# Kernel tuning notes

Hardware: AMD Instinct MI355X
Metric: run time of the kernel (lower is better)

The kernel has to match this reference:

```python
import jax, jax.numpy as jnp
import numpy as np

NUM_EXPERTS = 8
HIDDEN = 2048
INTER = 4096
TOKENS = 8192
TOP_K = 2


def setup_inputs() -> dict:
    key = jax.random.key(0)
    ks = jax.random.split(key, 5)
    s = 0.02
    return {
        "x": jax.random.normal(ks[0], (TOKENS, HIDDEN), dtype=jnp.float32),
        "gate_w": jax.random.normal(ks[1], (NUM_EXPERTS, HIDDEN), dtype=jnp.float32) * s,
        "w1": jax.random.normal(ks[2], (NUM_EXPERTS, INTER, HIDDEN), dtype=jnp.float32) * s,
        "w2": jax.random.normal(ks[3], (NUM_EXPERTS, HIDDEN, INTER), dtype=jnp.float32) * s,
        "w3": jax.random.normal(ks[4], (NUM_EXPERTS, INTER, HIDDEN), dtype=jnp.float32) * s,
    }


def reference(x, gate_w, w1, w2, w3):
    # Router: softmax over experts in fp32, then top-2 (no renormalization,
    # matching the torch module which uses the raw top-k softmax probs).
    router_logits = jnp.einsum("th,eh->te", x, gate_w)  # [T, E]
    probs = jax.nn.softmax(router_logits.astype(jnp.float32), axis=1)
    topk_w, topk_idx = jax.lax.top_k(probs, TOP_K)  # [T, K]
    topk_w = topk_w.astype(x.dtype)

    num_experts = w1.shape[0]
    out = jnp.zeros_like(x)
    for e in range(num_experts):
        # Combined routing coefficient for expert e per token (0 if unrouted).
        coef = jnp.sum(jnp.where(topk_idx == e, topk_w, 0.0), axis=1)  # [T]
        # SwiGLU expert FFN: down(silu(gate(x)) * up(x))
        g = jnp.einsum("th,ih->ti", x, w1[e])
        u = jnp.einsum("th,ih->ti", x, w3[e])
        h = jax.nn.silu(g) * u
        y = jnp.einsum("ti,hi->th", h, w2[e])
        out = out + coef[:, None] * y
    return out
```

## Files before the change

kernel.cpp:

```cpp
#include <hip/hip_runtime.h>
#include <stdint.h>
#include <stddef.h>


constexpr int kTokens  = 8192;
constexpr int kHidden  = 2048;
constexpr int kInter   = 4096;
constexpr int kExperts = 8;

constexpr int BM = 128, BN = 128, BK = 64;
constexpr int MAX_MT = (2 * kTokens) / BM + kExperts;

constexpr int BM2 = 256, BN2 = 128, BK2 = 64;
constexpr int MAX_MT2 = (2 * kTokens) / BM2 + kExperts;
constexpr int NT2 = kHidden / BK2;

typedef short bf16x8 __attribute__((ext_vector_type(8)));
typedef float f32x4  __attribute__((ext_vector_type(4)));
typedef unsigned int u32;

__device__ __forceinline__ unsigned short f2bf(float f) {
  union { float f; unsigned u; } v; v.f = f;
  unsigned r = v.u + 0x7FFFu + ((v.u >> 16) & 1u);
  return (unsigned short)(r >> 16);
}

__device__ __forceinline__ void gload16(const void* g, void* l) {
  __builtin_amdgcn_global_load_lds(
      (const __attribute__((address_space(1))) u32*)g,
      (__attribute__((address_space(3))) u32*)l, 16, 0, 0);
}

__global__ __launch_bounds__(256) void convert_w(
    const float* __restrict__ src, unsigned short* __restrict__ dst,
    int lp, int lq, int K, long nchunks)
{
  long stride = (long)gridDim.x * blockDim.x;
  for (long g = blockIdx.x * (long)blockDim.x + threadIdx.x; g < nchunks; g += stride) {
    int  l   = (int)(g & 1023);
    long blk = g >> 10;
    int  q   = (int)(blk & ((1 << lq) - 1));
    long ep  = blk >> lq;
    int  p   = (int)(ep & ((1 << lp) - 1));
    int  e   = (int)(ep >> lp);
    int r = l >> 3, cs = l & 7, c = cs ^ (r & 7);
    size_t soff = (((size_t)(e << lp) + p) * 128 + r) * (size_t)K + (size_t)q * 64 + c * 8;
    float4 v0 = *reinterpret_cast<const float4*>(src + soff);
    float4 v1 = *reinterpret_cast<const float4*>(src + soff + 4);
    uint4 o;
    o.x = (u32)f2bf(v0.x) | ((u32)f2bf(v0.y) << 16);
    o.y = (u32)f2bf(v0.z) | ((u32)f2bf(v0.w) << 16);
    o.z = (u32)f2bf(v1.x) | ((u32)f2bf(v1.y) << 16);
    o.w = (u32)f2bf(v1.z) | ((u32)f2bf(v1.w) << 16);
    *reinterpret_cast<uint4*>(dst + g * 8) = o;
  }
}

__global__ __launch_bounds__(256) void moe_router(
    const float* __restrict__ x, const float* __restrict__ gate_w,
    unsigned short* __restrict__ xb, int* __restrict__ counts,
    int* __restrict__ list_idx, float* __restrict__ list_w)
{
  const int lane = threadIdx.x & 63;
  const int wave = threadIdx.x >> 6;
  const int t = blockIdx.x * 4 + wave;

  float acc[kExperts];
#pragma unroll
  for (int e = 0; e < kExperts; ++e) acc[e] = 0.f;

  const float4* xrow = reinterpret_cast<const float4*>(x + (size_t)t * kHidden);
#pragma unroll
  for (int j = 0; j < 8; ++j) {
    float4 xv = xrow[j * 64 + lane];
    uint2 pk;
    pk.x = (u32)f2bf(xv.x) | ((u32)f2bf(xv.y) << 16);
    pk.y = (u32)f2bf(xv.z) | ((u32)f2bf(xv.w) << 16);
    *reinterpret_cast<uint2*>(xb + (size_t)t * kHidden + j * 256 + lane * 4) = pk;
#pragma unroll
    for (int e = 0; e < kExperts; ++e) {
      float4 gv = reinterpret_cast<const float4*>(gate_w + (size_t)e * kHidden)[j * 64 + lane];
      acc[e] += xv.x * gv.x + xv.y * gv.y + xv.z * gv.z + xv.w * gv.w;
    }
  }
#pragma unroll
  for (int e = 0; e < kExperts; ++e) {
#pragma unroll
    for (int m = 32; m >= 1; m >>= 1) acc[e] += __shfl_xor(acc[e], m);
  }
  if (lane == 0) {
    float mx = acc[0];
#pragma unroll
    for (int e = 1; e < kExperts; ++e) mx = fmaxf(mx, acc[e]);
    float p[kExperts]; float s = 0.f;
#pragma unroll
    for (int e = 0; e < kExperts; ++e) { p[e] = __expf(acc[e] - mx); s += p[e]; }
    float inv = 1.f / s;
    int i1 = 0; float v1 = p[0];
#pragma unroll
    for (int e = 1; e < kExperts; ++e) if (p[e] > v1) { v1 = p[e]; i1 = e; }
    int i2 = (i1 == 0) ? 1 : 0; float v2 = p[i2];
#pragma unroll
    for (int e = 0; e < kExperts; ++e) {
      if (e == i1 || e == i2) continue;
      if (p[e] > v2) { v2 = p[e]; i2 = e; }
    }
    int s1 = atomicAdd(&counts[i1], 1);
    list_idx[i1 * kTokens + s1] = t;
    list_w [i1 * kTokens + s1] = v1 * inv;
    int s2 = atomicAdd(&counts[i2], 1);
    list_idx[i2 * kTokens + s2] = t;
    list_w [i2 * kTokens + s2] = v2 * inv;
  }
}

__device__ __forceinline__ bool map_tile(const int* __restrict__ counts, int mt,
                                         int& e, int& lm, int& sb, int& ne)
{
  int tb = 0; sb = 0;
  for (e = 0; e < kExperts; ++e) {
    ne = counts[e];
    int tiles = (ne + BM - 1) / BM;
    if (mt < tb + tiles) { lm = mt - tb; return true; }
    tb += tiles; sb += ne;
  }
  return false;
}

__device__ __forceinline__ bool map_tile2(const int* __restrict__ counts, int mt,
                                          int& e, int& lm, int& sb, int& ne)
{
  int tb = 0; sb = 0;
  for (e = 0; e < kExperts; ++e) {
    ne = counts[e];
    int tiles = (ne + BM2 - 1) / BM2;
    if (mt < tb + tiles) { lm = mt - tb; return true; }
    tb += tiles; sb += ne;
  }
  return false;
}

__global__ __launch_bounds__(512, 2) void moe_gu2(
    const unsigned short* __restrict__ xb,
    const unsigned short* __restrict__ w1b, const unsigned short* __restrict__ w3b,
    const int* __restrict__ counts, const int* __restrict__ list_idx,
    unsigned short* __restrict__ hbuf)
{
  __shared__ unsigned short lds[65536];
  __shared__ int toks[BM2];

  const int tid = threadIdx.x;
  const int nt  = blockIdx.x / MAX_MT2;
  const int mt  = blockIdx.x % MAX_MT2;

  int e, lm, sb, ne;
  if (!map_tile2(counts, mt, e, lm, sb, ne)) return;
  const int row0 = lm * BM2;

  if (tid < BM2) {
    int lr = row0 + tid;
    toks[tid] = list_idx[e * kTokens + ((lr < ne) ? lr : 0)];
  }
  __syncthreads();

  const int lane = tid & 63;
  const int w    = tid >> 6;
  const int wr   = w >> 2;
  const int wc   = w & 3;

  const unsigned short* srcA[2][2];
  const unsigned short* srcB1[2];
  const unsigned short* srcB3[2];
  {
    const size_t bb = ((size_t)(e * (kInter / BN2) + nt) * (kHidden / BK2)) * 1024;
#pragma unroll
    for (int i = 0; i < 2; ++i) {
      int l = (w * 2 + i) * 64 + lane;
      int r = l >> 3, cs = l & 7, c = cs ^ (r & 7);
#pragma unroll
      for (int h = 0; h < 2; ++h)
        srcA[h][i] = xb + (size_t)toks[h * 128 + r] * kHidden + c * 8;
      srcB1[i] = w1b + (bb + l) * 8;
      srcB3[i] = w3b + (bb + l) * 8;
    }
  }

  f32x4 accG[8][2], accU[8][2];
  const f32x4 zero = {0.f, 0.f, 0.f, 0.f};
#pragma unroll
  for (int m = 0; m < 8; ++m)
#pragma unroll
    for (int n = 0; n < 2; ++n) { accG[m][n] = zero; accU[m][n] = zero; }

#pragma unroll
  for (int i = 0; i < 2; ++i) gload16(srcA[0][i], &lds[0 * 8192 + (w * 2 + i) * 512]);
#pragma unroll
  for (int i = 0; i < 2; ++i) gload16(srcA[1][i], &lds[1 * 8192 + (w * 2 + i) * 512]);
#pragma unroll
  for (int i = 0; i < 2; ++i) gload16(srcB1[i], &lds[32768 + (w * 2 + i) * 512]);
#pragma unroll
  for (int i = 0; i < 2; ++i) gload16(srcB3[i], &lds[49152 + (w * 2 + i) * 512]);
  asm volatile("s_waitcnt vmcnt(2)" ::: "memory");
  __builtin_amdgcn_sched_barrier(0);
  __builtin_amdgcn_s_barrier();

  for (int t = 0; t < NT2; ++t) {
    const int cb = t & 1, nb = cb ^ 1;
    const int tn = (t + 1 < NT2) ? (t + 1) : (NT2 - 1);
    const int Acur = (cb * 2 + wr) * 8192;
    const int B1c  = 32768 + cb * 8192;
    const int B3c  = 49152 + cb * 8192;
    const int An0  = (nb * 2 + 0) * 8192;
    const int An1  = (nb * 2 + 1) * 8192;
    const int B1n  = 32768 + nb * 8192;
    const int B3n  = 49152 + nb * 8192;

    bf16x8 a0[4][2], a1[4][2];
    {
      bf16x8 b1f[2][2];
#pragma unroll
      for (int m = 0; m < 4; ++m) {
        const int r = m * 16 + (lane & 15);
#pragma unroll
        for (int kk = 0; kk < 2; ++kk) {
          const int cq = kk * 4 + (lane >> 4);
          a0[m][kk] = *reinterpret_cast<const bf16x8*>(&lds[Acur + r * 64 + ((cq ^ (r & 7)) << 3)]);
        }
      }
#pragma unroll
      for (int n = 0; n < 2; ++n) {
        const int r = wc * 32 + n * 16 + (lane & 15);
#pragma unroll
        for (int kk = 0; kk < 2; ++kk) {
          const int cq = kk * 4 + (lane >> 4);
          b1f[n][kk] = *reinterpret_cast<const bf16x8*>(&lds[B1c + r * 64 + ((cq ^ (r & 7)) << 3)]);
        }
      }
#pragma unroll
      for (int i = 0; i < 2; ++i) gload16(srcA[0][i] + tn * 64, &lds[An0 + (w * 2 + i) * 512]);
      __builtin_amdgcn_s_setprio(1);
#pragma unroll
      for (int m = 0; m < 4; ++m)
#pragma unroll
        for (int n = 0; n < 2; ++n)
#pragma unroll
          for (int kk = 0; kk < 2; ++kk)
            accG[m][n] = __builtin_amdgcn_mfma_f32_16x16x32_bf16(a0[m][kk], b1f[n][kk], accG[m][n], 0, 0, 0);
      __builtin_amdgcn_s_setprio(0);
      __builtin_amdgcn_sched_barrier(0);
      __builtin_amdgcn_s_barrier();

#pragma unroll
      for (int m = 0; m < 4; ++m) {
        const int r = 64 + m * 16 + (lane & 15);
#pragma unroll
        for (int kk = 0; kk < 2; ++kk) {
          const int cq = kk * 4 + (lane >> 4);
          a1[m][kk] = *reinterpret_cast<const bf16x8*>(&lds[Acur + r * 64 + ((cq ^ (r & 7)) << 3)]);
        }
      }
#pragma unroll
      for (int i = 0; i < 2; ++i) gload16(srcA[1][i] + tn * 64, &lds[An1 + (w * 2 + i) * 512]);
      __builtin_amdgcn_s_setprio(1);
#pragma unroll
      for (int m = 0; m < 4; ++m)
#pragma unroll
        for (int n = 0; n < 2; ++n)
#pragma unroll
          for (int kk = 0; kk < 2; ++kk)
            accG[4 + m][n] = __builtin_amdgcn_mfma_f32_16x16x32_bf16(a1[m][kk], b1f[n][kk], accG[4 + m][n], 0, 0, 0);
      __builtin_amdgcn_s_setprio(0);
      __builtin_amdgcn_sched_barrier(0);
      asm volatile("s_waitcnt vmcnt(4)" ::: "memory");
      __builtin_amdgcn_s_barrier();
    }
    {
      bf16x8 b3f[2][2];
#pragma unroll
      for (int n = 0; n < 2; ++n) {
        const int r = wc * 32 + n * 16 + (lane & 15);
#pragma unroll
        for (int kk = 0; kk < 2; ++kk) {
          const int cq = kk * 4 + (lane >> 4);
          b3f[n][kk] = *reinterpret_cast<const bf16x8*>(&lds[B3c + r * 64 + ((cq ^ (r & 7)) << 3)]);
        }
      }
#pragma unroll
      for (int i = 0; i < 2; ++i) gload16(srcB1[i] + (size_t)tn * 8192, &lds[B1n + (w * 2 + i) * 512]);
      __builtin_amdgcn_s_setprio(1);
#pragma unroll
      for (int m = 0; m < 4; ++m)
#pragma unroll
        for (int n = 0; n < 2; ++n)
#pragma unroll
          for (int kk = 0; kk < 2; ++kk)
            accU[m][n] = __builtin_amdgcn_mfma_f32_16x16x32_bf16(a0[m][kk], b3f[n][kk], accU[m][n], 0, 0, 0);
      __builtin_amdgcn_s_setprio(0);
      __builtin_amdgcn_sched_barrier(0);
      __builtin_amdgcn_s_barrier();

#pragma unroll
      for (int i = 0; i < 2; ++i) gload16(srcB3[i] + (size_t)tn * 8192, &lds[B3n + (w * 2 + i) * 512]);
      __builtin_amdgcn_s_setprio(1);
#pragma unroll
      for (int m = 0; m < 4; ++m)
#pragma unroll
        for (int n = 0; n < 2; ++n)
#pragma unroll
          for (int kk = 0; kk < 2; ++kk)
            accU[4 + m][n] = __builtin_amdgcn_mfma_f32_16x16x32_bf16(a1[m][kk], b3f[n][kk], accU[4 + m][n], 0, 0, 0);
      __builtin_amdgcn_s_setprio(0);
      __builtin_amdgcn_sched_barrier(0);
      asm volatile("s_waitcnt vmcnt(2)" ::: "memory");
      __builtin_amdgcn_s_barrier();
    }
  }

#pragma unroll
  for (int am = 0; am < 8; ++am) {
#pragma unroll
    for (int r = 0; r < 4; ++r) {
      int rloc = wr * 128 + am * 16 + ((lane >> 4) * 4) + r;
      int lrow = row0 + rloc;
      if (lrow < ne) {
        size_t base = (size_t)(sb + lrow) * kInter + (size_t)nt * BN2 + wc * 32 + (lane & 15);
#pragma unroll
        for (int n = 0; n < 2; ++n) {
          float g = accG[am][n][r];
          float u = accU[am][n][r];
          float hv = (g / (1.f + __expf(-g))) * u;
          hbuf[base + n * 16] = f2bf(hv);
        }
      }
    }
  }
}

__global__ __launch_bounds__(256, 3) void moe_y(
    const unsigned short* __restrict__ hbuf,
    const unsigned short* __restrict__ w2b,
    const int* __restrict__ counts, const int* __restrict__ list_idx,
    const float* __restrict__ list_w,
    float* __restrict__ out)
{
  __shared__ unsigned short As[BM * BK];
  __shared__ unsigned short Bs[BN * BK];
  __shared__ int   toks[BM];
  __shared__ float cofs[BM];

  const int tid = threadIdx.x;
  const int nt  = blockIdx.x / MAX_MT;
  const int mt  = blockIdx.x % MAX_MT;

  int e, lm, sb, ne;
  if (!map_tile(counts, mt, e, lm, sb, ne)) return;
  const int row0 = lm * BM;

  if (tid < BM) {
    int lr = row0 + tid;
    bool v = lr < ne;
    toks[tid] = v ? list_idx[e * kTokens + lr] : 0;
    cofs[tid] = v ? list_w [e * kTokens + lr] : 0.f;
  }
  __syncthreads();

  const int lane = tid & 63;
  const int w = tid >> 6;
  const int wr = w >> 1, wc = w & 1;

  const unsigned short* srcA[4];
  const unsigned short* srcB2[4];
  const size_t bbase = ((size_t)(e * (kHidden / BN) + nt) * (kInter / BK)) * 1024;
#pragma unroll
  for (int i = 0; i < 4; ++i) {
    int l = (w * 4 + i) * 64 + lane;
    int r = l >> 3, cs = l & 7, c = cs ^ (r & 7);
    srcA[i]  = hbuf + (size_t)(sb + row0 + r) * kInter + c * 8;
    srcB2[i] = w2b  + (bbase + l) * 8;
  }

  f32x4 acc[4][4];
  const f32x4 zero = {0.f, 0.f, 0.f, 0.f};
#pragma unroll
  for (int m = 0; m < 4; ++m)
#pragma unroll
    for (int n = 0; n < 4; ++n) acc[m][n] = zero;

  for (int ks = 0; ks < kInter / BK; ++ks) {
#pragma unroll
    for (int i = 0; i < 4; ++i) {
      gload16(srcA[i]  + ks * BK,           &As[(w * 4 + i) * 512]);
      gload16(srcB2[i] + (size_t)ks * 8192, &Bs[(w * 4 + i) * 512]);
    }
    __syncthreads();
#pragma unroll
    for (int kk = 0; kk < 2; ++kk) {
      const int cq = kk * 4 + (lane >> 4);
      bf16x8 a[4], b[4];
#pragma unroll
      for (int m = 0; m < 4; ++m) {
        int row = wr * 64 + m * 16 + (lane & 15);
        a[m] = *reinterpret_cast<const bf16x8*>(&As[row * 64 + ((cq ^ (row & 7)) << 3)]);
      }
#pragma unroll
      for (int n = 0; n < 4; ++n) {
        int row = wc * 64 + n * 16 + (lane & 15);
        b[n] = *reinterpret_cast<const bf16x8*>(&Bs[row * 64 + ((cq ^ (row & 7)) << 3)]);
      }
#pragma unroll
      for (int m = 0; m < 4; ++m)
#pragma unroll
        for (int n = 0; n < 4; ++n)
          acc[m][n] = __builtin_amdgcn_mfma_f32_16x16x32_bf16(a[m], b[n], acc[m][n], 0, 0, 0);
    }
    __syncthreads();
  }

#pragma unroll
  for (int m = 0; m < 4; ++m) {
#pragma unroll
    for (int r = 0; r < 4; ++r) {
      int rloc = wr * 64 + m * 16 + ((lane >> 4) * 4) + r;
      if (row0 + rloc < ne) {
        float cf = cofs[rloc];
        size_t obase = (size_t)toks[rloc] * kHidden + (size_t)nt * BN + wc * 64 + (lane & 15);
#pragma unroll
        for (int n = 0; n < 4; ++n)
          atomicAdd(&out[obase + n * 16], cf * acc[m][n][r]);
      }
    }
  }
}

__global__ __launch_bounds__(256, 2) void moe_gu_f32(
    const unsigned short* __restrict__ xb,
    const float* __restrict__ w1, const float* __restrict__ w3,
    const int* __restrict__ counts, const int* __restrict__ list_idx,
    unsigned short* __restrict__ hbuf)
{
  __shared__ unsigned short As [BM * BK];
  __shared__ unsigned short B1s[BN * BK];
  __shared__ unsigned short B3s[BN * BK];
  __shared__ int toks[BM];

  const int tid = threadIdx.x;
  const int nt  = blockIdx.x / MAX_MT;
  const int mt  = blockIdx.x % MAX_MT;

  int e, lm, sb, ne;
  if (!map_tile(counts, mt, e, lm, sb, ne)) return;
  const int row0 = lm * BM;

  if (tid < BM) {
    int lr = row0 + tid;
    toks[tid] = list_idx[e * kTokens + ((lr < ne) ? lr : 0)];
  }
  __syncthreads();

  const unsigned short* aptr[4];
#pragma unroll
  for (int i = 0; i < 4; ++i) {
    int chunk = i * 256 + tid;
    int r = chunk >> 3, c8 = chunk & 7;
    aptr[i] = xb + (size_t)toks[r] * kHidden + c8 * 8;
  }
  const float* w1e = w1 + (size_t)e * kInter * kHidden;
  const float* w3e = w3 + (size_t)e * kInter * kHidden;

  f32x4 accG[4][4], accU[4][4];
  const f32x4 zero = {0.f, 0.f, 0.f, 0.f};
#pragma unroll
  for (int m = 0; m < 4; ++m)
#pragma unroll
    for (int n = 0; n < 4; ++n) { accG[m][n] = zero; accU[m][n] = zero; }

  const int lane = tid & 63;
  const int wr = (tid >> 6) >> 1;
  const int wc = (tid >> 6) & 1;

  for (int k0 = 0; k0 < kHidden; k0 += BK) {
#pragma unroll
    for (int i = 0; i < 4; ++i) {
      int chunk = i * 256 + tid;
      uint4 v = *reinterpret_cast<const uint4*>(aptr[i] + k0);
      *reinterpret_cast<uint4*>(&As[chunk * 8]) = v;
    }
#pragma unroll
    for (int i = 0; i < 8; ++i) {
      int c = i * 256 + tid;
      int rowB = c >> 4, c16 = c & 15;
      size_t off = ((size_t)(nt * BN + rowB)) * kHidden + k0 + c16 * 4;
      float4 v1 = *reinterpret_cast<const float4*>(w1e + off);
      float4 v3 = *reinterpret_cast<const float4*>(w3e + off);
      uint2 p1, p3;
      p1.x = (u32)f2bf(v1.x) | ((u32)f2bf(v1.y) << 16);
      p1.y = (u32)f2bf(v1.z) | ((u32)f2bf(v1.w) << 16);
      p3.x = (u32)f2bf(v3.x) | ((u32)f2bf(v3.y) << 16);
      p3.y = (u32)f2bf(v3.z) | ((u32)f2bf(v3.w) << 16);
      *reinterpret_cast<uint2*>(&B1s[rowB * BK + c16 * 4]) = p1;
      *reinterpret_cast<uint2*>(&B3s[rowB * BK + c16 * 4]) = p3;
    }
    __syncthreads();
#pragma unroll
    for (int kk = 0; kk < 2; ++kk) {
      const int klo = kk * 32 + (lane >> 4) * 8;
      bf16x8 a[4], b1v[4], b3v[4];
#pragma unroll
      for (int m = 0; m < 4; ++m)
        a[m] = *reinterpret_cast<const bf16x8*>(&As[(wr * 64 + m * 16 + (lane & 15)) * BK + klo]);
#pragma unroll
      for (int n = 0; n < 4; ++n) {
        b1v[n] = *reinterpret_cast<const bf16x8*>(&B1s[(wc * 64 + n * 16 + (lane & 15)) * BK + klo]);
        b3v[n] = *reinterpret_cast<const bf16x8*>(&B3s[(wc * 64 + n * 16 + (lane & 15)) * BK + klo]);
      }
#pragma unroll
      for (int m = 0; m < 4; ++m)
#pragma unroll
        for (int n = 0; n < 4; ++n) {
          accG[m][n] = __builtin_amdgcn_mfma_f32_16x16x32_bf16(a[m], b1v[n], accG[m][n], 0, 0, 0);
          accU[m][n] = __builtin_amdgcn_mfma_f32_16x16x32_bf16(a[m], b3v[n], accU[m][n], 0, 0, 0);
        }
    }
    __syncthreads();
  }
#pragma unroll
  for (int m = 0; m < 4; ++m) {
#pragma unroll
    for (int r = 0; r < 4; ++r) {
      int rloc = wr * 64 + m * 16 + ((lane >> 4) * 4) + r;
      int lrow = row0 + rloc;
      if (lrow < ne) {
        size_t base = (size_t)(sb + lrow) * kInter + (size_t)nt * BN + wc * 64 + (lane & 15);
#pragma unroll
        for (int n = 0; n < 4; ++n) {
          float g = accG[m][n][r];
          float u = accU[m][n][r];
          hbuf[base + n * 16] = f2bf((g / (1.f + __expf(-g))) * u);
        }
      }
    }
  }
}

__global__ __launch_bounds__(256, 2) void moe_y_f32(
    const unsigned short* __restrict__ hbuf,
    const float* __restrict__ w2,
    const int* __restrict__ counts, const int* __restrict__ list_idx,
    const float* __restrict__ list_w,
    float* __restrict__ out)
{
  __shared__ unsigned short As[BM * BK];
  __shared__ unsigned short Bs[BN * BK];
  __shared__ int   toks[BM];
  __shared__ float cofs[BM];

  const int tid = threadIdx.x;
  const int nt  = blockIdx.x / MAX_MT;
  const int mt  = blockIdx.x % MAX_MT;

  int e, lm, sb, ne;
  if (!map_tile(counts, mt, e, lm, sb, ne)) return;
  const int row0 = lm * BM;

  if (tid < BM) {
    int lr = row0 + tid;
    bool v = lr < ne;
    toks[tid] = v ? list_idx[e * kTokens + lr] : 0;
    cofs[tid] = v ? list_w [e * kTokens + lr] : 0.f;
  }
  __syncthreads();

  const float* w2e = w2 + (size_t)e * kHidden * kInter;
  const unsigned short* arow = hbuf + (size_t)(sb + row0) * kInter;

  f32x4 acc[4][4];
  const f32x4 zero = {0.f, 0.f, 0.f, 0.f};
#pragma unroll
  for (int m = 0; m < 4; ++m)
#pragma unroll
    for (int n = 0; n < 4; ++n) acc[m][n] = zero;

  const int lane = tid & 63;
  const int wr = (tid >> 6) >> 1;
  const int wc = (tid >> 6) & 1;

  for (int k0 = 0; k0 < kInter; k0 += BK) {
#pragma unroll
    for (int i = 0; i < 4; ++i) {
      int chunk = i * 256 + tid;
      int r = chunk >> 3, c8 = chunk & 7;
      uint4 v = *reinterpret_cast<const uint4*>(arow + (size_t)r * kInter + k0 + c8 * 8);
      *reinterpret_cast<uint4*>(&As[chunk * 8]) = v;
    }
#pragma unroll
    for (int i = 0; i < 8; ++i) {
      int c = i * 256 + tid;
      int rowB = c >> 4, c16 = c & 15;
      size_t off = ((size_t)(nt * BN + rowB)) * kInter + k0 + c16 * 4;
      float4 v2 = *reinterpret_cast<const float4*>(w2e + off);
      uint2 p2;
      p2.x = (u32)f2bf(v2.x) | ((u32)f2bf(v2.y) << 16);
      p2.y = (u32)f2bf(v2.z) | ((u32)f2bf(v2.w) << 16);
      *reinterpret_cast<uint2*>(&Bs[rowB * BK + c16 * 4]) = p2;
    }
    __syncthreads();
#pragma unroll
    for (int kk = 0; kk < 2; ++kk) {
      const int klo = kk * 32 + (lane >> 4) * 8;
      bf16x8 a[4], b[4];
#pragma unroll
      for (int m = 0; m < 4; ++m)
        a[m] = *reinterpret_cast<const bf16x8*>(&As[(wr * 64 + m * 16 + (lane & 15)) * BK + klo]);
#pragma unroll
      for (int n = 0; n < 4; ++n)
        b[n] = *reinterpret_cast<const bf16x8*>(&Bs[(wc * 64 + n * 16 + (lane & 15)) * BK + klo]);
#pragma unroll
      for (int m = 0; m < 4; ++m)
#pragma unroll
        for (int n = 0; n < 4; ++n)
          acc[m][n] = __builtin_amdgcn_mfma_f32_16x16x32_bf16(a[m], b[n], acc[m][n], 0, 0, 0);
    }
    __syncthreads();
  }
#pragma unroll
  for (int m = 0; m < 4; ++m) {
#pragma unroll
    for (int r = 0; r < 4; ++r) {
      int rloc = wr * 64 + m * 16 + ((lane >> 4) * 4) + r;
      if (row0 + rloc < ne) {
        float cf = cofs[rloc];
        size_t obase = (size_t)toks[rloc] * kHidden + (size_t)nt * BN + wc * 64 + (lane & 15);
#pragma unroll
        for (int n = 0; n < 4; ++n)
          atomicAdd(&out[obase + n * 16], cf * acc[m][n][r]);
      }
    }
  }
}

extern "C" void kernel_launch(void* const* d_in, const int* in_sizes, int n_in,
                              void* d_out, int out_size, void* d_ws, size_t ws_size,
                              hipStream_t stream)
{
  const float* x      = (const float*)d_in[0];
  const float* gate_w = (const float*)d_in[1];
  const float* w1     = (const float*)d_in[2];
  const float* w2     = (const float*)d_in[3];
  const float* w3     = (const float*)d_in[4];
  float* out = (float*)d_out;

  char* ws = (char*)d_ws;
  const size_t MiB = 1ull << 20;
  int*   counts   = (int*)(ws);
  int*   list_idx = (int*)(ws + 1024);
  float* list_w   = (float*)(ws + 1024 + kExperts * kTokens * 4);

  hipMemsetAsync(counts, 0, 1024, stream);
  hipMemsetAsync(out, 0, (size_t)kTokens * kHidden * sizeof(float), stream);

  if (ws_size >= 418 * MiB) {
    unsigned short* xb   = (unsigned short*)(ws + 1 * MiB);
    unsigned short* w1b  = (unsigned short*)(ws + 33 * MiB);
    unsigned short* w3b  = (unsigned short*)(ws + 161 * MiB);
    unsigned short* hbuf = (unsigned short*)(ws + 289 * MiB);
    unsigned short* w2b  = w1b;

    const long nch = (long)kExperts * (kInter / BN) * (kHidden / BK) * 1024;
    convert_w<<<4096, 256, 0, stream>>>(w1, w1b, 5, 5, kHidden, nch);
    convert_w<<<4096, 256, 0, stream>>>(w3, w3b, 5, 5, kHidden, nch);
    moe_router<<<kTokens / 4, 256, 0, stream>>>(x, gate_w, xb, counts, list_idx, list_w);
    moe_gu2<<<(kInter / BN2) * MAX_MT2, 512, 0, stream>>>(xb, w1b, w3b, counts, list_idx, hbuf);
    convert_w<<<4096, 256, 0, stream>>>(w2, w2b, 4, 6, kInter, nch);
    moe_y<<<(kHidden / BN) * MAX_MT, 256, 0, stream>>>(hbuf, w2b, counts, list_idx, list_w, out);
  } else {
    unsigned short* xb   = (unsigned short*)(ws + 1 * MiB);
    unsigned short* hbuf = (unsigned short*)(ws + 36 * MiB);
    moe_router<<<kTokens / 4, 256, 0, stream>>>(x, gate_w, xb, counts, list_idx, list_w);
    moe_gu_f32<<<(kInter / BN) * MAX_MT, 256, 0, stream>>>(xb, w1, w3, counts, list_idx, hbuf);
    moe_y_f32 <<<(kHidden / BN) * MAX_MT, 256, 0, stream>>>(hbuf, w2, counts, list_idx, list_w, out);
  }
}
```

Baseline: 1.492 ms.

## Restructure gate/up and down-projection kernels with staggered prefetch pipeline and larger down tiles

```diff
diff --git a/kernel.cpp b/kernel.cpp
--- a/kernel.cpp
+++ b/kernel.cpp
@@ -11,9 +11,13 @@
 constexpr int BM = 128, BN = 128, BK = 64;
 constexpr int MAX_MT = (2 * kTokens) / BM + kExperts;
 
-constexpr int BM2 = 256, BN2 = 128, BK2 = 64;
+constexpr int BM2 = 256;
 constexpr int MAX_MT2 = (2 * kTokens) / BM2 + kExperts;
-constexpr int NT2 = kHidden / BK2;
+constexpr int NT2 = kHidden / BK;
+constexpr int NTY = kInter / BK;
+constexpr int NPAN_GU = kInter / 128;
+constexpr int NPAN_Y  = kHidden / 256;
+constexpr int kSlotCap = 16512;
 
 typedef short bf16x8 __attribute__((ext_vector_type(8)));
 typedef float f32x4  __attribute__((ext_vector_type(4)));
@@ -30,6 +34,11 @@
       (const __attribute__((address_space(1))) u32*)g,
       (__attribute__((address_space(3))) u32*)l, 16, 0, 0);
 }
+
+#define SB0()    __builtin_amdgcn_sched_barrier(0)
+#define BAR()    __builtin_amdgcn_s_barrier()
+#define LGKM0()  asm volatile("s_waitcnt lgkmcnt(0)" ::: "memory")
+#define VM(N)    asm volatile("s_waitcnt vmcnt(" #N ")" ::: "memory")
 
 __global__ __launch_bounds__(256) void convert_w(
     const float* __restrict__ src, unsigned short* __restrict__ dst,
@@ -140,7 +149,7 @@
   return false;
 }
 
-__global__ __launch_bounds__(512, 2) void moe_gu2(
+__global__ __launch_bounds__(512, 2) void moe_gu4(
     const unsigned short* __restrict__ xb,
     const unsigned short* __restrict__ w1b, const unsigned short* __restrict__ w3b,
     const int* __restrict__ counts, const int* __restrict__ list_idx,
@@ -169,21 +178,18 @@
   const int wc   = w & 3;
 
   const unsigned short* srcA[2][2];
-  const unsigned short* srcB1[2];
-  const unsigned short* srcB3[2];
-  {
-    const size_t bb = ((size_t)(e * (kInter / BN2) + nt) * (kHidden / BK2)) * 1024;
-#pragma unroll
-    for (int i = 0; i < 2; ++i) {
-      int l = (w * 2 + i) * 64 + lane;
-      int r = l >> 3, cs = l & 7, c = cs ^ (r & 7);
-#pragma unroll
-      for (int h = 0; h < 2; ++h)
-        srcA[h][i] = xb + (size_t)toks[h * 128 + r] * kHidden + c * 8;
-      srcB1[i] = w1b + (bb + l) * 8;
-      srcB3[i] = w3b + (bb + l) * 8;
-    }
-  }
+  int cOff[2];
+#pragma unroll
+  for (int j = 0; j < 2; ++j) {
+    int l = (w * 2 + j) * 64 + lane;
+    int r = l >> 3, c = (l & 7) ^ (r & 7);
+#pragma unroll
+    for (int h = 0; h < 2; ++h)
+      srcA[h][j] = xb + (size_t)toks[h * 128 + r] * kHidden + c * 8;
+    cOff[j] = l * 8;
+  }
+  const unsigned short* pB1 = w1b + (size_t)(e * NPAN_GU + nt) * NT2 * 8192;
+  const unsigned short* pB3 = w3b + (size_t)(e * NPAN_GU + nt) * NT2 * 8192;
 
   f32x4 accG[8][2], accU[8][2];
   const f32x4 zero = {0.f, 0.f, 0.f, 0.f};
@@ -192,52 +198,57 @@
 #pragma unroll
     for (int n = 0; n < 2; ++n) { accG[m][n] = zero; accU[m][n] = zero; }
 
-#pragma unroll
-  for (int i = 0; i < 2; ++i) gload16(srcA[0][i], &lds[0 * 8192 + (w * 2 + i) * 512]);
-#pragma unroll
-  for (int i = 0; i < 2; ++i) gload16(srcA[1][i], &lds[1 * 8192 + (w * 2 + i) * 512]);
-#pragma unroll
-  for (int i = 0; i < 2; ++i) gload16(srcB1[i], &lds[32768 + (w * 2 + i) * 512]);
-#pragma unroll
-  for (int i = 0; i < 2; ++i) gload16(srcB3[i], &lds[49152 + (w * 2 + i) * 512]);
-  asm volatile("s_waitcnt vmcnt(2)" ::: "memory");
-  __builtin_amdgcn_sched_barrier(0);
-  __builtin_amdgcn_s_barrier();
-
-  for (int t = 0; t < NT2; ++t) {
-    const int cb = t & 1, nb = cb ^ 1;
-    const int tn = (t + 1 < NT2) ? (t + 1) : (NT2 - 1);
-    const int Acur = (cb * 2 + wr) * 8192;
-    const int B1c  = 32768 + cb * 8192;
-    const int B3c  = 49152 + cb * 8192;
-    const int An0  = (nb * 2 + 0) * 8192;
-    const int An1  = (nb * 2 + 1) * 8192;
-    const int B1n  = 32768 + nb * 8192;
-    const int B3n  = 49152 + nb * 8192;
-
-    bf16x8 a0[4][2], a1[4][2];
-    {
-      bf16x8 b1f[2][2];
+  const int dA = (w * 2) * 512;
+
+#pragma unroll
+  for (int j = 0; j < 2; ++j) gload16(pB1 + cOff[j], &lds[32768 + dA + j * 512]);
+#pragma unroll
+  for (int j = 0; j < 2; ++j) gload16(pB3 + cOff[j], &lds[49152 + dA + j * 512]);
+#pragma unroll
+  for (int j = 0; j < 2; ++j) gload16(srcA[0][j], &lds[0 + dA + j * 512]);
+#pragma unroll
+  for (int j = 0; j < 2; ++j) gload16(srcA[1][j], &lds[8192 + dA + j * 512]);
+#pragma unroll
+  for (int j = 0; j < 2; ++j) gload16(srcA[0][j] + BK, &lds[16384 + dA + j * 512]);
+#pragma unroll
+  for (int j = 0; j < 2; ++j) gload16(srcA[1][j] + BK, &lds[24576 + dA + j * 512]);
+  SB0(); VM(4); SB0(); BAR();
+
+  for (int s2 = 0; s2 < NT2; s2 += 2) {
+#pragma unroll
+    for (int u = 0; u < 2; ++u) {
+      const int s  = s2 + u;
+      const int b  = u, nb = u ^ 1;
+      const int sp1 = (s + 1 < NT2) ? (s + 1) : (NT2 - 1);
+      const int sp2 = (s + 2 < NT2) ? (s + 2) : (NT2 - 1);
+      const int aub = b * 16384 + wr * 8192;
+      const int b1b = 32768 + b * 8192;
+      const int b3b = 49152 + b * 8192;
+
+      bf16x8 a0[4][2], a1[4][2], b1f[2][2], b3f[2][2];
+
 #pragma unroll
       for (int m = 0; m < 4; ++m) {
-        const int r = m * 16 + (lane & 15);
+        const int rr = m * 16 + (lane & 15);
 #pragma unroll
         for (int kk = 0; kk < 2; ++kk) {
           const int cq = kk * 4 + (lane >> 4);
-          a0[m][kk] = *reinterpret_cast<const bf16x8*>(&lds[Acur + r * 64 + ((cq ^ (r & 7)) << 3)]);
+          a0[m][kk] = *reinterpret_cast<const bf16x8*>(&lds[aub + rr * 64 + ((cq ^ (rr & 7)) << 3)]);
         }
       }
 #pragma unroll
       for (int n = 0; n < 2; ++n) {
-        const int r = wc * 32 + n * 16 + (lane & 15);
+        const int rr = wc * 32 + n * 16 + (lane & 15);
 #pragma unroll
         for (int kk = 0; kk < 2; ++kk) {
           const int cq = kk * 4 + (lane >> 4);
-          b1f[n][kk] = *reinterpret_cast<const bf16x8*>(&lds[B1c + r * 64 + ((cq ^ (r & 7)) << 3)]);
-        }
-      }
-#pragma unroll
-      for (int i = 0; i < 2; ++i) gload16(srcA[0][i] + tn * 64, &lds[An0 + (w * 2 + i) * 512]);
+          b1f[n][kk] = *reinterpret_cast<const bf16x8*>(&lds[b1b + rr * 64 + ((cq ^ (rr & 7)) << 3)]);
+        }
+      }
+#pragma unroll
+      for (int j = 0; j < 2; ++j)
+        gload16(pB1 + (size_t)sp1 * 8192 + cOff[j], &lds[32768 + nb * 8192 + dA + j * 512]);
+      SB0(); BAR(); LGKM0(); SB0();
       __builtin_amdgcn_s_setprio(1);
 #pragma unroll
       for (int m = 0; m < 4; ++m)
@@ -247,20 +258,21 @@
           for (int kk = 0; kk < 2; ++kk)
             accG[m][n] = __builtin_amdgcn_mfma_f32_16x16x32_bf16(a0[m][kk], b1f[n][kk], accG[m][n], 0, 0, 0);
       __builtin_amdgcn_s_setprio(0);
-      __builtin_amdgcn_sched_barrier(0);
-      __builtin_amdgcn_s_barrier();
+      SB0(); BAR();
 
 #pragma unroll
       for (int m = 0; m < 4; ++m) {
-        const int r = 64 + m * 16 + (lane & 15);
+        const int rr = 64 + m * 16 + (lane & 15);
 #pragma unroll
         for (int kk = 0; kk < 2; ++kk) {
           const int cq = kk * 4 + (lane >> 4);
-          a1[m][kk] = *reinterpret_cast<const bf16x8*>(&lds[Acur + r * 64 + ((cq ^ (r & 7)) << 3)]);
-        }
-      }
-#pragma unroll
-      for (int i = 0; i < 2; ++i) gload16(srcA[1][i] + tn * 64, &lds[An1 + (w * 2 + i) * 512]);
+          a1[m][kk] = *reinterpret_cast<const bf16x8*>(&lds[aub + rr * 64 + ((cq ^ (rr & 7)) << 3)]);
+        }
+      }
+#pragma unroll
+      for (int j = 0; j < 2; ++j)
+        gload16(pB3 + (size_t)sp1 * 8192 + cOff[j], &lds[49152 + nb * 8192 + dA + j * 512]);
+      SB0(); BAR(); LGKM0(); SB0();
       __builtin_amdgcn_s_setprio(1);
 #pragma unroll
       for (int m = 0; m < 4; ++m)
@@ -270,23 +282,21 @@
           for (int kk = 0; kk < 2; ++kk)
             accG[4 + m][n] = __builtin_amdgcn_mfma_f32_16x16x32_bf16(a1[m][kk], b1f[n][kk], accG[4 + m][n], 0, 0, 0);
       __builtin_amdgcn_s_setprio(0);
-      __builtin_amdgcn_sched_barrier(0);
-      asm volatile("s_waitcnt vmcnt(4)" ::: "memory");
-      __builtin_amdgcn_s_barrier();
-    }
-    {
-      bf16x8 b3f[2][2];
+      SB0(); VM(8); BAR();
+
 #pragma unroll
       for (int n = 0; n < 2; ++n) {
-        const int r = wc * 32 + n * 16 + (lane & 15);
+        const int rr = wc * 32 + n * 16 + (lane & 15);
 #pragma unroll
         for (int kk = 0; kk < 2; ++kk) {
           const int cq = kk * 4 + (lane >> 4);
-          b3f[n][kk] = *reinterpret_cast<const bf16x8*>(&lds[B3c + r * 64 + ((cq ^ (r & 7)) << 3)]);
-        }
-      }
-#pragma unroll
-      for (int i = 0; i < 2; ++i) gload16(srcB1[i] + (size_t)tn * 8192, &lds[B1n + (w * 2 + i) * 512]);
+          b3f[n][kk] = *reinterpret_cast<const bf16x8*>(&lds[b3b + rr * 64 + ((cq ^ (rr & 7)) << 3)]);
+        }
+      }
+#pragma unroll
+      for (int j = 0; j < 2; ++j)
+        gload16(srcA[0][j] + sp2 * BK, &lds[b * 16384 + dA + j * 512]);
+      SB0(); BAR(); LGKM0(); SB0();
       __builtin_amdgcn_s_setprio(1);
 #pragma unroll
       for (int m = 0; m < 4; ++m)
@@ -296,11 +306,12 @@
           for (int kk = 0; kk < 2; ++kk)
             accU[m][n] = __builtin_amdgcn_mfma_f32_16x16x32_bf16(a0[m][kk], b3f[n][kk], accU[m][n], 0, 0, 0);
       __builtin_amdgcn_s_setprio(0);
-      __builtin_amdgcn_sched_barrier(0);
-      __builtin_amdgcn_s_barrier();
-
-#pragma unroll
-      for (int i = 0; i < 2; ++i) gload16(srcB3[i] + (size_t)tn * 8192, &lds[B3n + (w * 2 + i) * 512]);
+      SB0(); BAR();
+
+#pragma unroll
+      for (int j = 0; j < 2; ++j)
+        gload16(srcA[1][j] + sp2 * BK, &lds[b * 16384 + 8192 + dA + j * 512]);
+      SB0(); BAR(); LGKM0(); SB0();
       __builtin_amdgcn_s_setprio(1);
 #pragma unroll
       for (int m = 0; m < 4; ++m)
@@ -310,9 +321,7 @@
           for (int kk = 0; kk < 2; ++kk)
             accU[4 + m][n] = __builtin_amdgcn_mfma_f32_16x16x32_bf16(a1[m][kk], b3f[n][kk], accU[4 + m][n], 0, 0, 0);
       __builtin_amdgcn_s_setprio(0);
-      __builtin_amdgcn_sched_barrier(0);
-      asm volatile("s_waitcnt vmcnt(2)" ::: "memory");
-      __builtin_amdgcn_s_barrier();
+      SB0(); VM(6); BAR();
     }
   }
 
@@ -323,7 +332,7 @@
       int rloc = wr * 128 + am * 16 + ((lane >> 4) * 4) + r;
       int lrow = row0 + rloc;
       if (lrow < ne) {
-        size_t base = (size_t)(sb + lrow) * kInter + (size_t)nt * BN2 + wc * 32 + (lane & 15);
+        size_t base = (size_t)(sb + lrow) * kInter + (size_t)nt * 128 + wc * 32 + (lane & 15);
 #pragma unroll
         for (int n = 0; n < 2; ++n) {
           float g = accG[am][n][r];
@@ -336,27 +345,26 @@
   }
 }
 
-__global__ __launch_bounds__(256, 3) void moe_y(
+__global__ __launch_bounds__(512, 2) void moe_y4(
     const unsigned short* __restrict__ hbuf,
     const unsigned short* __restrict__ w2b,
     const int* __restrict__ counts, const int* __restrict__ list_idx,
     const float* __restrict__ list_w,
     float* __restrict__ out)
 {
-  __shared__ unsigned short As[BM * BK];
-  __shared__ unsigned short Bs[BN * BK];
-  __shared__ int   toks[BM];
-  __shared__ float cofs[BM];
+  __shared__ unsigned short lds[65536];
+  __shared__ int   toks[BM2];
+  __shared__ float cofs[BM2];
 
   const int tid = threadIdx.x;
-  const int nt  = blockIdx.x / MAX_MT;
-  const int mt  = blockIdx.x % MAX_MT;
+  const int nt  = blockIdx.x / MAX_MT2;
+  const int mt  = blockIdx.x % MAX_MT2;
 
   int e, lm, sb, ne;
-  if (!map_tile(counts, mt, e, lm, sb, ne)) return;
-  const int row0 = lm * BM;
-
-  if (tid < BM) {
+  if (!map_tile2(counts, mt, e, lm, sb, ne)) return;
+  const int row0 = lm * BM2;
+
+  if (tid < BM2) {
     int lr = row0 + tid;
     bool v = lr < ne;
     toks[tid] = v ? list_idx[e * kTokens + lr] : 0;
@@ -365,68 +373,175 @@
   __syncthreads();
 
   const int lane = tid & 63;
-  const int w = tid >> 6;
-  const int wr = w >> 1, wc = w & 1;
-
-  const unsigned short* srcA[4];
-  const unsigned short* srcB2[4];
-  const size_t bbase = ((size_t)(e * (kHidden / BN) + nt) * (kInter / BK)) * 1024;
-#pragma unroll
-  for (int i = 0; i < 4; ++i) {
-    int l = (w * 4 + i) * 64 + lane;
-    int r = l >> 3, cs = l & 7, c = cs ^ (r & 7);
-    srcA[i]  = hbuf + (size_t)(sb + row0 + r) * kInter + c * 8;
-    srcB2[i] = w2b  + (bbase + l) * 8;
-  }
-
-  f32x4 acc[4][4];
+  const int w    = tid >> 6;
+  const int wr   = w >> 2;
+  const int wc   = w & 3;
+
+  const unsigned short* srcA[2][2];
+  int cOff[2];
+#pragma unroll
+  for (int j = 0; j < 2; ++j) {
+    int l = (w * 2 + j) * 64 + lane;
+    int r = l >> 3, c = (l & 7) ^ (r & 7);
+#pragma unroll
+    for (int h = 0; h < 2; ++h) {
+      int rg = sb + row0 + h * 128 + r;
+      if (rg > kSlotCap - 1) rg = kSlotCap - 1;
+      srcA[h][j] = hbuf + (size_t)rg * kInter + c * 8;
+    }
+    cOff[j] = l * 8;
+  }
+  const unsigned short* pB[2];
+#pragma unroll
+  for (int h = 0; h < 2; ++h)
+    pB[h] = w2b + (size_t)(e * 16 + nt * 2 + h) * NTY * 8192;
+
+  f32x4 acc[8][4];
   const f32x4 zero = {0.f, 0.f, 0.f, 0.f};
 #pragma unroll
-  for (int m = 0; m < 4; ++m)
+  for (int m = 0; m < 8; ++m)
 #pragma unroll
     for (int n = 0; n < 4; ++n) acc[m][n] = zero;
 
-  for (int ks = 0; ks < kInter / BK; ++ks) {
-#pragma unroll
-    for (int i = 0; i < 4; ++i) {
-      gload16(srcA[i]  + ks * BK,           &As[(w * 4 + i) * 512]);
-      gload16(srcB2[i] + (size_t)ks * 8192, &Bs[(w * 4 + i) * 512]);
-    }
-    __syncthreads();
-#pragma unroll
-    for (int kk = 0; kk < 2; ++kk) {
-      const int cq = kk * 4 + (lane >> 4);
-      bf16x8 a[4], b[4];
+  const int dA = (w * 2) * 512;
+  const int bwh = wc >> 1;
+  const int brr0 = (wc & 1) * 64;
+
+#pragma unroll
+  for (int j = 0; j < 2; ++j) gload16(pB[0] + cOff[j], &lds[32768 + dA + j * 512]);
+#pragma unroll
+  for (int j = 0; j < 2; ++j) gload16(pB[1] + cOff[j], &lds[40960 + dA + j * 512]);
+#pragma unroll
+  for (int j = 0; j < 2; ++j) gload16(srcA[0][j], &lds[0 + dA + j * 512]);
+#pragma unroll
+  for (int j = 0; j < 2; ++j) gload16(srcA[1][j], &lds[8192 + dA + j * 512]);
+#pragma unroll
+  for (int j = 0; j < 2; ++j) gload16(srcA[0][j] + BK, &lds[16384 + dA + j * 512]);
+#pragma unroll
+  for (int j = 0; j < 2; ++j) gload16(srcA[1][j] + BK, &lds[24576 + dA + j * 512]);
+  SB0(); VM(4); SB0(); BAR();
+
+  for (int s2 = 0; s2 < NTY; s2 += 2) {
+#pragma unroll
+    for (int u = 0; u < 2; ++u) {
+      const int s  = s2 + u;
+      const int b  = u, nb = u ^ 1;
+      const int sp1 = (s + 1 < NTY) ? (s + 1) : (NTY - 1);
+      const int sp2 = (s + 2 < NTY) ? (s + 2) : (NTY - 1);
+      const int aub = b * 16384 + wr * 8192;
+      const int bub = 32768 + b * 16384 + bwh * 8192;
+
+      bf16x8 a0[4][2], a1[4][2], b01[2][2], b23[2][2];
+
 #pragma unroll
       for (int m = 0; m < 4; ++m) {
-        int row = wr * 64 + m * 16 + (lane & 15);
-        a[m] = *reinterpret_cast<const bf16x8*>(&As[row * 64 + ((cq ^ (row & 7)) << 3)]);
-      }
-#pragma unroll
-      for (int n = 0; n < 4; ++n) {
-        int row = wc * 64 + n * 16 + (lane & 15);
-        b[n] = *reinterpret_cast<const bf16x8*>(&Bs[row * 64 + ((cq ^ (row & 7)) << 3)]);
-      }
-#pragma unroll
-      for (int m = 0; m < 4; ++m)
-#pragma unroll
-        for (int n = 0; n < 4; ++n)
-          acc[m][n] = __builtin_amdgcn_mfma_f32_16x16x32_bf16(a[m], b[n], acc[m][n], 0, 0, 0);
-    }
-    __syncthreads();
-  }
-
-#pragma unroll
-  for (int m = 0; m < 4; ++m) {
+        const int rr = m * 16 + (lane & 15);
+#pragma unroll
+        for (int kk = 0; kk < 2; ++kk) {
+          const int cq = kk * 4 + (lane >> 4);
+          a0[m][kk] = *reinterpret_cast<const bf16x8*>(&lds[aub + rr * 64 + ((cq ^ (rr & 7)) << 3)]);
+        }
+      }
+#pragma unroll
+      for (int n = 0; n < 2; ++n) {
+        const int rr = brr0 + n * 16 + (lane & 15);
+#pragma unroll
+        for (int kk = 0; kk < 2; ++kk) {
+          const int cq = kk * 4 + (lane >> 4);
+          b01[n][kk] = *reinterpret_cast<const bf16x8*>(&lds[bub + rr * 64 + ((cq ^ (rr & 7)) << 3)]);
+        }
+      }
+#pragma unroll
+      for (int j = 0; j < 2; ++j)
+        gload16(pB[0] + (size_t)sp1 * 8192 + cOff[j], &lds[32768 + nb * 16384 + dA + j * 512]);
+      SB0(); BAR(); LGKM0(); SB0();
+      __builtin_amdgcn_s_setprio(1);
+#pragma unroll
+      for (int m = 0; m < 4; ++m)
+#pragma unroll
+        for (int n = 0; n < 2; ++n)
+#pragma unroll
+          for (int kk = 0; kk < 2; ++kk)
+            acc[m][n] = __builtin_amdgcn_mfma_f32_16x16x32_bf16(a0[m][kk], b01[n][kk], acc[m][n], 0, 0, 0);
+      __builtin_amdgcn_s_setprio(0);
+      SB0(); BAR();
+
+#pragma unroll
+      for (int m = 0; m < 4; ++m) {
+        const int rr = 64 + m * 16 + (lane & 15);
+#pragma unroll
+        for (int kk = 0; kk < 2; ++kk) {
+          const int cq = kk * 4 + (lane >> 4);
+          a1[m][kk] = *reinterpret_cast<const bf16x8*>(&lds[aub + rr * 64 + ((cq ^ (rr & 7)) << 3)]);
+        }
+      }
+#pragma unroll
+      for (int j = 0; j < 2; ++j)
+        gload16(pB[1] + (size_t)sp1 * 8192 + cOff[j], &lds[40960 + nb * 16384 + dA + j * 512]);
+      SB0(); BAR(); LGKM0(); SB0();
+      __builtin_amdgcn_s_setprio(1);
+#pragma unroll
+      for (int m = 0; m < 4; ++m)
+#pragma unroll
+        for (int n = 0; n < 2; ++n)
+#pragma unroll
+          for (int kk = 0; kk < 2; ++kk)
+            acc[4 + m][n] = __builtin_amdgcn_mfma_f32_16x16x32_bf16(a1[m][kk], b01[n][kk], acc[4 + m][n], 0, 0, 0);
+      __builtin_amdgcn_s_setprio(0);
+      SB0(); BAR();
+
+#pragma unroll
+      for (int n = 0; n < 2; ++n) {
+        const int rr = brr0 + 32 + n * 16 + (lane & 15);
+#pragma unroll
+        for (int kk = 0; kk < 2; ++kk) {
+          const int cq = kk * 4 + (lane >> 4);
+          b23[n][kk] = *reinterpret_cast<const bf16x8*>(&lds[bub + rr * 64 + ((cq ^ (rr & 7)) << 3)]);
+        }
+      }
+#pragma unroll
+      for (int j = 0; j < 2; ++j)
+        gload16(srcA[0][j] + sp2 * BK, &lds[b * 16384 + dA + j * 512]);
+      SB0(); BAR(); LGKM0(); SB0();
+      __builtin_amdgcn_s_setprio(1);
+#pragma unroll
+      for (int m = 0; m < 4; ++m)
+#pragma unroll
+        for (int n = 0; n < 2; ++n)
+#pragma unroll
+          for (int kk = 0; kk < 2; ++kk)
+            acc[m][2 + n] = __builtin_amdgcn_mfma_f32_16x16x32_bf16(a0[m][kk], b23[n][kk], acc[m][2 + n], 0, 0, 0);
+      __builtin_amdgcn_s_setprio(0);
+      SB0(); BAR();
+
+#pragma unroll
+      for (int j = 0; j < 2; ++j)
+        gload16(srcA[1][j] + sp2 * BK, &lds[b * 16384 + 8192 + dA + j * 512]);
+      SB0(); BAR(); LGKM0(); SB0();
+      __builtin_amdgcn_s_setprio(1);
+#pragma unroll
+      for (int m = 0; m < 4; ++m)
+#pragma unroll
+        for (int n = 0; n < 2; ++n)
+#pragma unroll
+          for (int kk = 0; kk < 2; ++kk)
+            acc[4 + m][2 + n] = __builtin_amdgcn_mfma_f32_16x16x32_bf16(a1[m][kk], b23[n][kk], acc[4 + m][2 + n], 0, 0, 0);
+      __builtin_amdgcn_s_setprio(0);
+      SB0(); VM(4); BAR();
+    }
+  }
+
+#pragma unroll
+  for (int am = 0; am < 8; ++am) {
 #pragma unroll
     for (int r = 0; r < 4; ++r) {
-      int rloc = wr * 64 + m * 16 + ((lane >> 4) * 4) + r;
+      int rloc = wr * 128 + am * 16 + ((lane >> 4) * 4) + r;
       if (row0 + rloc < ne) {
         float cf = cofs[rloc];
-        size_t obase = (size_t)toks[rloc] * kHidden + (size_t)nt * BN + wc * 64 + (lane & 15);
+        size_t obase = (size_t)toks[rloc] * kHidden + (size_t)nt * 256 + wc * 64 + (lane & 15);
 #pragma unroll
         for (int n = 0; n < 4; ++n)
-          atomicAdd(&out[obase + n * 16], cf * acc[m][n][r]);
+          atomicAdd(&out[obase + n * 16], cf * acc[am][n][r]);
       }
     }
   }
@@ -665,13 +780,13 @@
     unsigned short* hbuf = (unsigned short*)(ws + 289 * MiB);
     unsigned short* w2b  = w1b;
 
-    const long nch = (long)kExperts * (kInter / BN) * (kHidden / BK) * 1024;
+    const long nch = (long)kExperts * 32 * 32 * 1024;
     convert_w<<<4096, 256, 0, stream>>>(w1, w1b, 5, 5, kHidden, nch);
     convert_w<<<4096, 256, 0, stream>>>(w3, w3b, 5, 5, kHidden, nch);
     moe_router<<<kTokens / 4, 256, 0, stream>>>(x, gate_w, xb, counts, list_idx, list_w);
-    moe_gu2<<<(kInter / BN2) * MAX_MT2, 512, 0, stream>>>(xb, w1b, w3b, counts, list_idx, hbuf);
+    moe_gu4<<<NPAN_GU * MAX_MT2, 512, 0, stream>>>(xb, w1b, w3b, counts, list_idx, hbuf);
     convert_w<<<4096, 256, 0, stream>>>(w2, w2b, 4, 6, kInter, nch);
-    moe_y<<<(kHidden / BN) * MAX_MT, 256, 0, stream>>>(hbuf, w2b, counts, list_idx, list_w, out);
+    moe_y4<<<NPAN_Y * MAX_MT2, 512, 0, stream>>>(hbuf, w2b, counts, list_idx, list_w, out);
   } else {
     unsigned short* xb   = (unsigned short*)(ws + 1 * MiB);
     unsigned short* hbuf = (unsigned short*)(ws + 36 * MiB);
```

After: 1.737 ms. 1.16x slower.
